# Kernel optimization log

Hardware: AMD Instinct MI355X
Metric: run time of the kernel (lower is better)

The kernel has to match this reference:

```python
import jax, jax.numpy as jnp
import numpy as np

EMB = 1024
HEADS = 8
HEAD_DIM = EMB // HEADS


def setup_inputs() -> dict:
    key = jax.random.key(0)
    ks = jax.random.split(key, 11)
    B, S = 4, 2048
    scale = 1.0 / np.sqrt(EMB)
    inp = {
        "query": jax.random.normal(ks[0], (B, S, EMB), jnp.float32),
        "key": jax.random.normal(ks[1], (B, S, EMB), jnp.float32),
        "value": jax.random.normal(ks[2], (B, S, EMB), jnp.float32),
        "Wq": jax.random.normal(ks[3], (EMB, EMB), jnp.float32) * scale,
        "bq": jnp.zeros((EMB,), jnp.float32),
        "Wk": jax.random.normal(ks[4], (EMB, EMB), jnp.float32) * scale,
        "bk": jnp.zeros((EMB,), jnp.float32),
        "Wv": jax.random.normal(ks[5], (EMB, EMB), jnp.float32) * scale,
        "bv": jnp.zeros((EMB,), jnp.float32),
        "Wo": jax.random.normal(ks[6], (EMB, EMB), jnp.float32) * scale,
        "bo": jnp.zeros((EMB,), jnp.float32),
    }
    return inp


def _split_heads(x):
    B, S, _ = x.shape
    return x.reshape(B, S, HEADS, HEAD_DIM).transpose(0, 2, 1, 3)  # [B,H,S,D]


def reference(query, key, value, Wq, bq, Wk, bk, Wv, bv, Wo, bo):
    Q = _split_heads(query @ Wq.T + bq)
    K = _split_heads(key @ Wk.T + bk)
    V = _split_heads(value @ Wv.T + bv)
    # [B,H,S,S] attention scores, scaled by sqrt(head_dim)
    scores = jnp.einsum("bhqd,bhkd->bhqk", Q, K) / jnp.sqrt(
        jnp.asarray(HEAD_DIM, Q.dtype)
    )
    attention = jax.nn.softmax(scores, axis=-1)
    # dropout is identity in eval mode
    x = jnp.einsum("bhqk,bhkd->bhqd", attention, V)
    B, H, S, D = x.shape
    x = x.transpose(0, 2, 1, 3).reshape(B, S, EMB)
    x = x @ Wo.T + bo
    return (x, attention)
```

## Files before the change

kernel.cpp:

```cpp
#include <hip/hip_runtime.h>
#include <hip/hip_bf16.h>
#include <math.h>

#define BB 4
#define SS 2048
#define EMB 1024
#define HH 8
#define DD 128

typedef __attribute__((ext_vector_type(8))) short bf16x8;
typedef __attribute__((ext_vector_type(4))) float f32x4;

__device__ __forceinline__ unsigned short f2bf(float f) {
    unsigned u = __builtin_bit_cast(unsigned, f);
    u += 0x7FFFu + ((u >> 16) & 1u);
    return (unsigned short)(u >> 16);
}

__device__ __forceinline__ void gload_lds16(const void* g, void* l) {
    __builtin_amdgcn_global_load_lds(
        (const __attribute__((address_space(1))) unsigned int*)g,
        (__attribute__((address_space(3))) unsigned int*)l, 16, 0, 0);
}

#define SB0 __builtin_amdgcn_sched_barrier(0)

__global__ void f2bf3_kernel(const float* __restrict__ a, const float* __restrict__ b,
                             const float* __restrict__ c, unsigned short* __restrict__ dst,
                             int n4) {
    const float* src = blockIdx.z == 0 ? a : (blockIdx.z == 1 ? b : c);
    unsigned short* d = dst + (size_t)blockIdx.z * ((size_t)n4 * 4);
    int i = blockIdx.x * blockDim.x + threadIdx.x;
    int stride = gridDim.x * blockDim.x;
    for (; i < n4; i += stride) {
        float4 f = ((const float4*)src)[i];
        ushort4 o;
        o.x = f2bf(f.x); o.y = f2bf(f.y); o.z = f2bf(f.z); o.w = f2bf(f.w);
        ((ushort4*)d)[i] = o;
    }
}

__global__ void f2bf4_kernel(const float* __restrict__ a, const float* __restrict__ b,
                             const float* __restrict__ c, const float* __restrict__ e,
                             unsigned short* __restrict__ dst, int n4) {
    const float* src = blockIdx.z == 0 ? a : (blockIdx.z == 1 ? b : (blockIdx.z == 2 ? c : e));
    unsigned short* d = dst + (size_t)blockIdx.z * ((size_t)n4 * 4);
    int i = blockIdx.x * blockDim.x + threadIdx.x;
    int stride = gridDim.x * blockDim.x;
    for (; i < n4; i += stride) {
        float4 f = ((const float4*)src)[i];
        ushort4 o;
        o.x = f2bf(f.x); o.y = f2bf(f.y); o.z = f2bf(f.z); o.w = f2bf(f.w);
        ((ushort4*)d)[i] = o;
    }
}

template <int MODE>
__device__ __forceinline__ void gemm_core(const unsigned short* __restrict__ A,
                                          const unsigned short* __restrict__ Bw,
                                          const float* __restrict__ bias,
                                          void* __restrict__ Cout, float scale)
{
    __shared__ short As[2][128 * 32];
    __shared__ short Bs[2][128 * 32];
    const int K = 1024;
    const int m0 = blockIdx.x * 128, n0 = blockIdx.y * 128;
    const int t = threadIdx.x;
    const int lane = t & 63, w = t >> 6;
    const int wr = w >> 1, wc = w & 1;
    const int g = lane >> 4, li = lane & 15;
    f32x4 acc[4][4] = {};

    auto stage = [&](int k0, int buf) {
        #pragma unroll
        for (int i = 0; i < 2; ++i) {
            int idx = i * 256 + t;
            int row = idx >> 2, col = (idx & 3) * 8;
            gload_lds16(A  + (size_t)(m0 + row) * K + k0 + col, &As[buf][idx * 8]);
            gload_lds16(Bw + (size_t)(n0 + row) * K + k0 + col, &Bs[buf][idx * 8]);
        }
    };

    stage(0, 0);
    for (int ki = 0; ki < 32; ++ki) {
        const int cur = ki & 1;
        if (ki < 31) {
            stage((ki + 1) * 32, cur ^ 1);
            asm volatile("s_waitcnt vmcnt(4)" ::: "memory");
        } else {
            asm volatile("s_waitcnt vmcnt(0)" ::: "memory");
        }
        SB0; __builtin_amdgcn_s_barrier(); SB0;

        bf16x8 af[4], bfr[4];
        #pragma unroll
        for (int mi = 0; mi < 4; ++mi)
            af[mi] = *(const bf16x8*)&As[cur][(wr * 64 + mi * 16 + li) * 32 + g * 8];
        #pragma unroll
        for (int ni = 0; ni < 4; ++ni)
            bfr[ni] = *(const bf16x8*)&Bs[cur][(wc * 64 + ni * 16 + li) * 32 + g * 8];
        #pragma unroll
        for (int mi = 0; mi < 4; ++mi) {
            #pragma unroll
            for (int ni = 0; ni < 4; ++ni)
                acc[mi][ni] = __builtin_amdgcn_mfma_f32_16x16x32_bf16(
                    af[mi], bfr[ni], acc[mi][ni], 0, 0, 0);
        }
        asm volatile("s_waitcnt lgkmcnt(0)" ::: "memory");
        SB0; __builtin_amdgcn_s_barrier(); SB0;
    }

    #pragma unroll
    for (int mi = 0; mi < 4; ++mi) {
        #pragma unroll
        for (int ni = 0; ni < 4; ++ni) {
            int n = n0 + wc * 64 + ni * 16 + li;
            float bv = bias[n];
            #pragma unroll
            for (int i = 0; i < 4; ++i) {
                int m = m0 + wr * 64 + mi * 16 + g * 4 + i;
                float v = acc[mi][ni][i] + bv;
                if (MODE == 0) {
                    v *= scale;
                    int b = m >> 11, s = m & 2047, h = n >> 7, d = n & 127;
                    ((unsigned short*)Cout)[((((size_t)b * HH + h) * SS + s) << 7) + d] = f2bf(v);
                } else {
                    ((float*)Cout)[(size_t)m * EMB + n] = v;
                }
            }
        }
    }
}

__global__ __launch_bounds__(256, 2)
void gemm_qkv(const unsigned short* __restrict__ XB, const unsigned short* __restrict__ WB,
              const float* __restrict__ bq, const float* __restrict__ bk,
              const float* __restrict__ bv, unsigned short* __restrict__ QKVb, float qscale)
{
    const size_t NX = (size_t)BB * SS * EMB;
    const size_t NW = (size_t)EMB * EMB;
    const int z = blockIdx.z;
    const float* bias = z == 0 ? bq : (z == 1 ? bk : bv);
    gemm_core<0>(XB + z * NX, WB + z * NW, bias, QKVb + z * NX, z == 0 ? qscale : 1.f);
}

__global__ __launch_bounds__(256, 2)
void gemm_out(const unsigned short* __restrict__ Ob, const unsigned short* __restrict__ Wo,
              const float* __restrict__ bo, float* __restrict__ outx)
{
    gemm_core<1>(Ob, Wo, bo, outx, 1.f);
}

__global__ __launch_bounds__(256, 2)
void attn_kernel(const unsigned short* __restrict__ Qb,
                 const unsigned short* __restrict__ Kb,
                 const unsigned short* __restrict__ Vb,
                 float* __restrict__ attn,
                 unsigned short* __restrict__ Ob)
{
    __shared__ short Ks[64 * 128];
    __shared__ short Vt[128 * 64];
    __shared__ short Ps[4][16 * 68];

    const int t = threadIdx.x;
    const int lane = t & 63, w = t >> 6;
    const int g = lane >> 4, li = lane & 15;
    const int bh = blockIdx.y;
    const int q0 = blockIdx.x * 64 + w * 16;

    const unsigned short* Kbh = Kb + (size_t)bh * SS * DD;
    const unsigned short* Vbh = Vb + (size_t)bh * SS * DD;

    bf16x8 qf[4];
    {
        const unsigned short* qp = Qb + ((size_t)bh * SS + q0 + li) * DD + g * 8;
        #pragma unroll
        for (int kk = 0; kk < 4; ++kk) qf[kk] = *(const bf16x8*)(qp + kk * 32);
    }

    float l_i[4] = {0.f, 0.f, 0.f, 0.f};

    auto stageK = [&](int kt2, char* dst) {
        const char* ksrc = (const char*)(Kbh + kt2 * 64 * DD);
        #pragma unroll
        for (int i = 0; i < 4; ++i) {
            int lb = (i * 256 + t) * 16;
            int row = lb >> 8;
            gload_lds16(ksrc + (lb ^ ((row & 7) << 4)), dst + lb);
        }
    };

    stageK(0, (char*)Ks);
    for (int kt = 0; kt < 32; ++kt) {
        const char* cur = (kt & 1) ? (const char*)Vt : (const char*)Ks;
        char* nxt = (kt & 1) ? (char*)Ks : (char*)Vt;
        if (kt < 31) {
            stageK(kt + 1, nxt);
            asm volatile("s_waitcnt vmcnt(4)" ::: "memory");
        } else {
            asm volatile("s_waitcnt vmcnt(0)" ::: "memory");
        }
        SB0; __builtin_amdgcn_s_barrier(); SB0;

        f32x4 sacc[4];
        #pragma unroll
        for (int kc = 0; kc < 4; ++kc) {
            f32x4 a = {0.f, 0.f, 0.f, 0.f};
            int row = kc * 16 + li;
            int sw = (row & 7) << 4;
            #pragma unroll
            for (int kk = 0; kk < 4; ++kk) {
                bf16x8 kf = *(const bf16x8*)(cur + row * 256 + ((kk * 64 + g * 16) ^ sw));
                a = __builtin_amdgcn_mfma_f32_16x16x32_bf16(qf[kk], kf, a, 0, 0, 0);
            }
            sacc[kc] = a;
        }
        #pragma unroll
        for (int i = 0; i < 4; ++i) {
            float ts = __builtin_amdgcn_exp2f(sacc[0][i]) + __builtin_amdgcn_exp2f(sacc[1][i])
                     + __builtin_amdgcn_exp2f(sacc[2][i]) + __builtin_amdgcn_exp2f(sacc[3][i]);
            #pragma unroll
            for (int mk = 1; mk < 16; mk <<= 1) ts += __shfl_xor(ts, mk, 64);
            l_i[i] += ts;
        }
        __builtin_amdgcn_s_barrier(); SB0;
    }

    float rl[4];
    #pragma unroll
    for (int i = 0; i < 4; ++i) rl[i] = 1.f / l_i[i];

    f32x4 O[8] = {};
    float* arow = attn + (size_t)bh * SS * SS;

    bf16x8 va[2], vbr[2];
    #pragma unroll
    for (int i = 0; i < 2; ++i) {
        int idx = i * 256 + t;
        int k0 = (idx >> 4) * 2, d0 = (idx & 15) * 8;
        va[i]  = *(const bf16x8*)(Vbh + k0 * DD + d0);
        vbr[i] = *(const bf16x8*)(Vbh + (k0 + 1) * DD + d0);
    }

    for (int kt = 0; kt < 32; ++kt) {
        __syncthreads();
        const char* ksrc = (const char*)(Kbh + kt * 64 * DD);
        #pragma unroll
        for (int i = 0; i < 4; ++i) {
            int lb = (i * 256 + t) * 16;
            int row = lb >> 8;
            gload_lds16(ksrc + (lb ^ ((row & 7) << 4)), (char*)Ks + lb);
        }
        #pragma unroll
        for (int i = 0; i < 2; ++i) {
            int idx = i * 256 + t;
            int kpair = idx >> 4, d0 = (idx & 15) * 8;
            #pragma unroll
            for (int j = 0; j < 8; ++j) {
                unsigned pk = (unsigned)(unsigned short)va[i][j]
                            | ((unsigned)(unsigned short)vbr[i][j] << 16);
                int d = d0 + j;
                int ba = (d * 128 + kpair * 4) ^ (((d >> 3) & 7) << 4);
                *(unsigned*)((char*)Vt + ba) = pk;
            }
        }
        __syncthreads();

        if (kt < 31) {
            const unsigned short* vn = Vbh + (kt + 1) * 64 * DD;
            #pragma unroll
            for (int i = 0; i < 2; ++i) {
                int idx = i * 256 + t;
                int k0 = (idx >> 4) * 2, d0 = (idx & 15) * 8;
                va[i]  = *(const bf16x8*)(vn + k0 * DD + d0);
                vbr[i] = *(const bf16x8*)(vn + (k0 + 1) * DD + d0);
            }
        }

        #pragma unroll
        for (int kc = 0; kc < 4; ++kc) {
            f32x4 a = {0.f, 0.f, 0.f, 0.f};
            int row = kc * 16 + li;
            int sw = (row & 7) << 4;
            #pragma unroll
            for (int kk = 0; kk < 4; ++kk) {
                bf16x8 kf = *(const bf16x8*)((const char*)Ks + row * 256 + ((kk * 64 + g * 16) ^ sw));
                a = __builtin_amdgcn_mfma_f32_16x16x32_bf16(qf[kk], kf, a, 0, 0, 0);
            }
            #pragma unroll
            for (int i = 0; i < 4; ++i) {
                float p = __builtin_amdgcn_exp2f(a[i]) * rl[i];
                int qr = g * 4 + i;
                __builtin_nontemporal_store(p, &arow[(size_t)(q0 + qr) * SS + kt * 64 + kc * 16 + li]);
                Ps[w][qr * 68 + kc * 16 + li] = (short)f2bf(p);
            }
        }
        asm volatile("s_waitcnt lgkmcnt(0)" ::: "memory");
        SB0;

        bf16x8 pf0 = *(const bf16x8*)&Ps[w][li * 68 + g * 8];
        bf16x8 pf1 = *(const bf16x8*)&Ps[w][li * 68 + 32 + g * 8];
        #pragma unroll
        for (int dt = 0; dt < 8; ++dt) {
            int dr = dt * 16 + li;
            int vsw = ((dr >> 3) & 7) << 4;
            bf16x8 vf0 = *(const bf16x8*)((const char*)Vt + dr * 128 + ((g * 16) ^ vsw));
            bf16x8 vf1 = *(const bf16x8*)((const char*)Vt + dr * 128 + ((64 + g * 16) ^ vsw));
            O[dt] = __builtin_amdgcn_mfma_f32_16x16x32_bf16(pf0, vf0, O[dt], 0, 0, 0);
            O[dt] = __builtin_amdgcn_mfma_f32_16x16x32_bf16(pf1, vf1, O[dt], 0, 0, 0);
        }
    }

    const int b = bh >> 3, h = bh & 7;
    #pragma unroll
    for (int dt = 0; dt < 8; ++dt) {
        #pragma unroll
        for (int i = 0; i < 4; ++i) {
            size_t r = (size_t)b * SS + q0 + g * 4 + i;
            Ob[r * EMB + h * DD + dt * 16 + li] = f2bf(O[dt][i]);
        }
    }
}

extern "C" void kernel_launch(void* const* d_in, const int* in_sizes, int n_in,
                              void* d_out, int out_size, void* d_ws, size_t ws_size,
                              hipStream_t stream)
{
    const float* q  = (const float*)d_in[0];
    const float* k  = (const float*)d_in[1];
    const float* v  = (const float*)d_in[2];
    const float* Wq = (const float*)d_in[3];
    const float* bq = (const float*)d_in[4];
    const float* Wk = (const float*)d_in[5];
    const float* bk = (const float*)d_in[6];
    const float* Wv = (const float*)d_in[7];
    const float* bv = (const float*)d_in[8];
    const float* Wo = (const float*)d_in[9];
    const float* bo = (const float*)d_in[10];

    const size_t NX = (size_t)BB * SS * EMB;
    const size_t NW = (size_t)EMB * EMB;

    unsigned short* Qb = (unsigned short*)d_ws;
    unsigned short* Ob = Qb + 3 * NX;
    unsigned short* WB = Ob + NX;

    float* outx = (float*)d_out;
    float* attn = outx + NX;
    unsigned short* XB = (unsigned short*)attn;

    f2bf3_kernel<<<dim3(1024, 1, 3), 256, 0, stream>>>(q, k, v, XB, (int)(NX / 4));
    f2bf4_kernel<<<dim3(128, 1, 4), 256, 0, stream>>>(Wq, Wk, Wv, Wo, WB, (int)(NW / 4));

    const float qscale = 1.4426950408889634f / sqrtf((float)DD);
    gemm_qkv<<<dim3(64, 8, 3), 256, 0, stream>>>(XB, WB, bq, bk, bv, Qb, qscale);

    attn_kernel<<<dim3(32, 32), 256, 0, stream>>>(Qb, Qb + NX, Qb + 2 * NX, attn, Ob);

    gemm_out<<<dim3(64, 8), 256, 0, stream>>>(Ob, WB + 3 * NW, bo, outx);
}
```

Before: 356.3 us.

## Process 32 query rows per wave in attention to reuse K/V tiles

Each wave now handles two 16-row query subtiles (128 queries per block), so every K and V tile staged in LDS feeds twice as many MFMAs, and the grid shrinks to 512 blocks. The softmax row sums are accumulated per lane and cross-lane reduced only once after the first pass, instead of every tile. Block ids are remapped so that consecutive blocks spread across batch-heads. This raises register pressure (more accumulators and Q fragments), which could hurt occupancy under the 2-blocks-per-SM launch bound.

```diff
diff --git a/kernel.cpp b/kernel.cpp
--- a/kernel.cpp
+++ b/kernel.cpp
@@ -160,25 +160,28 @@
 {
     __shared__ short Ks[64 * 128];
     __shared__ short Vt[128 * 64];
-    __shared__ short Ps[4][16 * 68];
+    __shared__ short Ps[4][32 * 68];
 
     const int t = threadIdx.x;
     const int lane = t & 63, w = t >> 6;
     const int g = lane >> 4, li = lane & 15;
-    const int bh = blockIdx.y;
-    const int q0 = blockIdx.x * 64 + w * 16;
+
+    const int id = blockIdx.x + blockIdx.y * 16;
+    const int bh = (id & 7) * 4 + ((id >> 3) & 3);
+    const int q0 = (id >> 5) * 128 + w * 32;
 
     const unsigned short* Kbh = Kb + (size_t)bh * SS * DD;
     const unsigned short* Vbh = Vb + (size_t)bh * SS * DD;
 
-    bf16x8 qf[4];
-    {
-        const unsigned short* qp = Qb + ((size_t)bh * SS + q0 + li) * DD + g * 8;
-        #pragma unroll
-        for (int kk = 0; kk < 4; ++kk) qf[kk] = *(const bf16x8*)(qp + kk * 32);
-    }
-
-    float l_i[4] = {0.f, 0.f, 0.f, 0.f};
+    bf16x8 qf[8];
+    #pragma unroll
+    for (int rh = 0; rh < 2; ++rh) {
+        const unsigned short* qp = Qb + ((size_t)bh * SS + q0 + rh * 16 + li) * DD + g * 8;
+        #pragma unroll
+        for (int kk = 0; kk < 4; ++kk) qf[rh * 4 + kk] = *(const bf16x8*)(qp + kk * 32);
+    }
+
+    float lacc[8] = {0.f, 0.f, 0.f, 0.f, 0.f, 0.f, 0.f, 0.f};
 
     auto stageK = [&](int kt2, char* dst) {
         const char* ksrc = (const char*)(Kbh + kt2 * 64 * DD);
@@ -202,35 +205,36 @@
         }
         SB0; __builtin_amdgcn_s_barrier(); SB0;
 
-        f32x4 sacc[4];
         #pragma unroll
         for (int kc = 0; kc < 4; ++kc) {
-            f32x4 a = {0.f, 0.f, 0.f, 0.f};
             int row = kc * 16 + li;
             int sw = (row & 7) << 4;
+            f32x4 a0 = {0.f, 0.f, 0.f, 0.f}, a1 = {0.f, 0.f, 0.f, 0.f};
             #pragma unroll
             for (int kk = 0; kk < 4; ++kk) {
                 bf16x8 kf = *(const bf16x8*)(cur + row * 256 + ((kk * 64 + g * 16) ^ sw));
-                a = __builtin_amdgcn_mfma_f32_16x16x32_bf16(qf[kk], kf, a, 0, 0, 0);
-            }
-            sacc[kc] = a;
-        }
-        #pragma unroll
-        for (int i = 0; i < 4; ++i) {
-            float ts = __builtin_amdgcn_exp2f(sacc[0][i]) + __builtin_amdgcn_exp2f(sacc[1][i])
-                     + __builtin_amdgcn_exp2f(sacc[2][i]) + __builtin_amdgcn_exp2f(sacc[3][i]);
-            #pragma unroll
-            for (int mk = 1; mk < 16; mk <<= 1) ts += __shfl_xor(ts, mk, 64);
-            l_i[i] += ts;
+                a0 = __builtin_amdgcn_mfma_f32_16x16x32_bf16(qf[kk],     kf, a0, 0, 0, 0);
+                a1 = __builtin_amdgcn_mfma_f32_16x16x32_bf16(qf[4 + kk], kf, a1, 0, 0, 0);
+            }
+            #pragma unroll
+            for (int i = 0; i < 4; ++i) {
+                lacc[i]     += __builtin_amdgcn_exp2f(a0[i]);
+                lacc[4 + i] += __builtin_amdgcn_exp2f(a1[i]);
+            }
         }
         __builtin_amdgcn_s_barrier(); SB0;
     }
 
-    float rl[4];
-    #pragma unroll
-    for (int i = 0; i < 4; ++i) rl[i] = 1.f / l_i[i];
-
-    f32x4 O[8] = {};
+    float rl[8];
+    #pragma unroll
+    for (int i = 0; i < 8; ++i) {
+        float ts = lacc[i];
+        #pragma unroll
+        for (int mk = 1; mk < 16; mk <<= 1) ts += __shfl_xor(ts, mk, 64);
+        rl[i] = 1.f / ts;
+    }
+
+    f32x4 O[16] = {};
     float* arow = attn + (size_t)bh * SS * SS;
 
     bf16x8 va[2], vbr[2];
@@ -279,20 +283,24 @@
 
         #pragma unroll
         for (int kc = 0; kc < 4; ++kc) {
-            f32x4 a = {0.f, 0.f, 0.f, 0.f};
             int row = kc * 16 + li;
             int sw = (row & 7) << 4;
+            f32x4 a0 = {0.f, 0.f, 0.f, 0.f}, a1 = {0.f, 0.f, 0.f, 0.f};
             #pragma unroll
             for (int kk = 0; kk < 4; ++kk) {
                 bf16x8 kf = *(const bf16x8*)((const char*)Ks + row * 256 + ((kk * 64 + g * 16) ^ sw));
-                a = __builtin_amdgcn_mfma_f32_16x16x32_bf16(qf[kk], kf, a, 0, 0, 0);
+                a0 = __builtin_amdgcn_mfma_f32_16x16x32_bf16(qf[kk],     kf, a0, 0, 0, 0);
+                a1 = __builtin_amdgcn_mfma_f32_16x16x32_bf16(qf[4 + kk], kf, a1, 0, 0, 0);
             }
             #pragma unroll
             for (int i = 0; i < 4; ++i) {
-                float p = __builtin_amdgcn_exp2f(a[i]) * rl[i];
-                int qr = g * 4 + i;
-                __builtin_nontemporal_store(p, &arow[(size_t)(q0 + qr) * SS + kt * 64 + kc * 16 + li]);
-                Ps[w][qr * 68 + kc * 16 + li] = (short)f2bf(p);
+                float p0 = __builtin_amdgcn_exp2f(a0[i]) * rl[i];
+                float p1 = __builtin_amdgcn_exp2f(a1[i]) * rl[4 + i];
+                int qr0 = g * 4 + i, qr1 = 16 + qr0;
+                __builtin_nontemporal_store(p0, &arow[(size_t)(q0 + qr0) * SS + kt * 64 + kc * 16 + li]);
+                __builtin_nontemporal_store(p1, &arow[(size_t)(q0 + qr1) * SS + kt * 64 + kc * 16 + li]);
+                Ps[w][qr0 * 68 + kc * 16 + li] = (short)f2bf(p0);
+                Ps[w][qr1 * 68 + kc * 16 + li] = (short)f2bf(p1);
             }
         }
         asm volatile("s_waitcnt lgkmcnt(0)" ::: "memory");
@@ -300,24 +308,31 @@
 
         bf16x8 pf0 = *(const bf16x8*)&Ps[w][li * 68 + g * 8];
         bf16x8 pf1 = *(const bf16x8*)&Ps[w][li * 68 + 32 + g * 8];
+        bf16x8 pf2 = *(const bf16x8*)&Ps[w][(16 + li) * 68 + g * 8];
+        bf16x8 pf3 = *(const bf16x8*)&Ps[w][(16 + li) * 68 + 32 + g * 8];
         #pragma unroll
         for (int dt = 0; dt < 8; ++dt) {
             int dr = dt * 16 + li;
             int vsw = ((dr >> 3) & 7) << 4;
             bf16x8 vf0 = *(const bf16x8*)((const char*)Vt + dr * 128 + ((g * 16) ^ vsw));
             bf16x8 vf1 = *(const bf16x8*)((const char*)Vt + dr * 128 + ((64 + g * 16) ^ vsw));
-            O[dt] = __builtin_amdgcn_mfma_f32_16x16x32_bf16(pf0, vf0, O[dt], 0, 0, 0);
-            O[dt] = __builtin_amdgcn_mfma_f32_16x16x32_bf16(pf1, vf1, O[dt], 0, 0, 0);
+            O[dt]     = __builtin_amdgcn_mfma_f32_16x16x32_bf16(pf0, vf0, O[dt],     0, 0, 0);
+            O[dt]     = __builtin_amdgcn_mfma_f32_16x16x32_bf16(pf1, vf1, O[dt],     0, 0, 0);
+            O[8 + dt] = __builtin_amdgcn_mfma_f32_16x16x32_bf16(pf2, vf0, O[8 + dt], 0, 0, 0);
+            O[8 + dt] = __builtin_amdgcn_mfma_f32_16x16x32_bf16(pf3, vf1, O[8 + dt], 0, 0, 0);
         }
     }
 
     const int b = bh >> 3, h = bh & 7;
     #pragma unroll
-    for (int dt = 0; dt < 8; ++dt) {
-        #pragma unroll
-        for (int i = 0; i < 4; ++i) {
-            size_t r = (size_t)b * SS + q0 + g * 4 + i;
-            Ob[r * EMB + h * DD + dt * 16 + li] = f2bf(O[dt][i]);
+    for (int rh = 0; rh < 2; ++rh) {
+        #pragma unroll
+        for (int dt = 0; dt < 8; ++dt) {
+            #pragma unroll
+            for (int i = 0; i < 4; ++i) {
+                size_t r = (size_t)b * SS + q0 + rh * 16 + g * 4 + i;
+                Ob[r * EMB + h * DD + dt * 16 + li] = f2bf(O[rh * 8 + dt][i]);
+            }
         }
     }
 }
@@ -355,7 +370,7 @@
     const float qscale = 1.4426950408889634f / sqrtf((float)DD);
     gemm_qkv<<<dim3(64, 8, 3), 256, 0, stream>>>(XB, WB, bq, bk, bv, Qb, qscale);
 
-    attn_kernel<<<dim3(32, 32), 256, 0, stream>>>(Qb, Qb + NX, Qb + 2 * NX, attn, Ob);
+    attn_kernel<<<dim3(16, 32), 256, 0, stream>>>(Qb, Qb + NX, Qb + 2 * NX, attn, Ob);
 
     gemm_out<<<dim3(64, 8), 256, 0, stream>>>(Ob, WB + 3 * NW, bo, outx);
 }
```

Result: slower. 379.9 us (+6.6%).

## Split softmax denominator pass into separate tiled QK^T sum-exp kernel

Applied to the files above, without the earlier changes.

Moves the first pass of attention, which computes the softmax row sums (sum of exp of QK^T), out of attn_kernel into a dedicated 128x128-tiled GEMM kernel. That kernel writes partial sums per column tile, and a small reduction kernel turns them into reciprocals. The large tiles give better MFMA reuse and more parallelism than the 16-row-per-wave streaming loop. The cost is two extra launches and a scratch buffer placed in the output region, which gemm_out later overwrites.

```diff
diff --git a/kernel.cpp b/kernel.cpp
--- a/kernel.cpp
+++ b/kernel.cpp
@@ -152,9 +152,91 @@
 }
 
 __global__ __launch_bounds__(256, 2)
+void qk_sumexp(const unsigned short* __restrict__ Qb,
+               const unsigned short* __restrict__ Kb,
+               float* __restrict__ lp)
+{
+    __shared__ short As[2][128 * 32];
+    __shared__ short Bs[2][128 * 32];
+    const int bh = blockIdx.z;
+    const int m0 = blockIdx.x * 128, n0 = blockIdx.y * 128;
+    const unsigned short* A  = Qb + (size_t)bh * SS * DD;
+    const unsigned short* Bw = Kb + (size_t)bh * SS * DD;
+    const int t = threadIdx.x;
+    const int lane = t & 63, w = t >> 6;
+    const int wr = w >> 1, wc = w & 1;
+    const int g = lane >> 4, li = lane & 15;
+    f32x4 acc[4][4] = {};
+
+    auto stage = [&](int k0, int buf) {
+        #pragma unroll
+        for (int i = 0; i < 2; ++i) {
+            int idx = i * 256 + t;
+            int row = idx >> 2, col = (idx & 3) * 8;
+            gload_lds16(A  + (size_t)(m0 + row) * DD + k0 + col, &As[buf][idx * 8]);
+            gload_lds16(Bw + (size_t)(n0 + row) * DD + k0 + col, &Bs[buf][idx * 8]);
+        }
+    };
+
+    stage(0, 0);
+    #pragma unroll
+    for (int ki = 0; ki < 4; ++ki) {
+        const int cur = ki & 1;
+        if (ki < 3) {
+            stage((ki + 1) * 32, cur ^ 1);
+            asm volatile("s_waitcnt vmcnt(4)" ::: "memory");
+        } else {
+            asm volatile("s_waitcnt vmcnt(0)" ::: "memory");
+        }
+        SB0; __builtin_amdgcn_s_barrier(); SB0;
+
+        bf16x8 af[4], bfr[4];
+        #pragma unroll
+        for (int mi = 0; mi < 4; ++mi)
+            af[mi] = *(const bf16x8*)&As[cur][(wr * 64 + mi * 16 + li) * 32 + g * 8];
+        #pragma unroll
+        for (int ni = 0; ni < 4; ++ni)
+            bfr[ni] = *(const bf16x8*)&Bs[cur][(wc * 64 + ni * 16 + li) * 32 + g * 8];
+        #pragma unroll
+        for (int mi = 0; mi < 4; ++mi) {
+            #pragma unroll
+            for (int ni = 0; ni < 4; ++ni)
+                acc[mi][ni] = __builtin_amdgcn_mfma_f32_16x16x32_bf16(
+                    af[mi], bfr[ni], acc[mi][ni], 0, 0, 0);
+        }
+        asm volatile("s_waitcnt lgkmcnt(0)" ::: "memory");
+        SB0; __builtin_amdgcn_s_barrier(); SB0;
+    }
+
+    #pragma unroll
+    for (int mi = 0; mi < 4; ++mi) {
+        #pragma unroll
+        for (int i = 0; i < 4; ++i) {
+            float s = __builtin_amdgcn_exp2f(acc[mi][0][i]) + __builtin_amdgcn_exp2f(acc[mi][1][i])
+                    + __builtin_amdgcn_exp2f(acc[mi][2][i]) + __builtin_amdgcn_exp2f(acc[mi][3][i]);
+            #pragma unroll
+            for (int mk = 1; mk < 16; mk <<= 1) s += __shfl_xor(s, mk, 64);
+            if (li == 0) {
+                int q = m0 + wr * 64 + mi * 16 + g * 4 + i;
+                lp[((size_t)bh * SS + q) * 32 + blockIdx.y * 2 + wc] = s;
+            }
+        }
+    }
+}
+
+__global__ void lred_kernel(const float* __restrict__ lp, float* __restrict__ rlg) {
+    int r = blockIdx.x * blockDim.x + threadIdx.x;
+    float s = 0.f;
+    #pragma unroll
+    for (int j = 0; j < 32; ++j) s += lp[(size_t)r * 32 + j];
+    rlg[r] = 1.f / s;
+}
+
+__global__ __launch_bounds__(256, 2)
 void attn_kernel(const unsigned short* __restrict__ Qb,
                  const unsigned short* __restrict__ Kb,
                  const unsigned short* __restrict__ Vb,
+                 const float* __restrict__ rlg,
                  float* __restrict__ attn,
                  unsigned short* __restrict__ Ob)
 {
@@ -178,57 +260,9 @@
         for (int kk = 0; kk < 4; ++kk) qf[kk] = *(const bf16x8*)(qp + kk * 32);
     }
 
-    float l_i[4] = {0.f, 0.f, 0.f, 0.f};
-
-    auto stageK = [&](int kt2, char* dst) {
-        const char* ksrc = (const char*)(Kbh + kt2 * 64 * DD);
-        #pragma unroll
-        for (int i = 0; i < 4; ++i) {
-            int lb = (i * 256 + t) * 16;
-            int row = lb >> 8;
-            gload_lds16(ksrc + (lb ^ ((row & 7) << 4)), dst + lb);
-        }
-    };
-
-    stageK(0, (char*)Ks);
-    for (int kt = 0; kt < 32; ++kt) {
-        const char* cur = (kt & 1) ? (const char*)Vt : (const char*)Ks;
-        char* nxt = (kt & 1) ? (char*)Ks : (char*)Vt;
-        if (kt < 31) {
-            stageK(kt + 1, nxt);
-            asm volatile("s_waitcnt vmcnt(4)" ::: "memory");
-        } else {
-            asm volatile("s_waitcnt vmcnt(0)" ::: "memory");
-        }
-        SB0; __builtin_amdgcn_s_barrier(); SB0;
-
-        f32x4 sacc[4];
-        #pragma unroll
-        for (int kc = 0; kc < 4; ++kc) {
-            f32x4 a = {0.f, 0.f, 0.f, 0.f};
-            int row = kc * 16 + li;
-            int sw = (row & 7) << 4;
-            #pragma unroll
-            for (int kk = 0; kk < 4; ++kk) {
-                bf16x8 kf = *(const bf16x8*)(cur + row * 256 + ((kk * 64 + g * 16) ^ sw));
-                a = __builtin_amdgcn_mfma_f32_16x16x32_bf16(qf[kk], kf, a, 0, 0, 0);
-            }
-            sacc[kc] = a;
-        }
-        #pragma unroll
-        for (int i = 0; i < 4; ++i) {
-            float ts = __builtin_amdgcn_exp2f(sacc[0][i]) + __builtin_amdgcn_exp2f(sacc[1][i])
-                     + __builtin_amdgcn_exp2f(sacc[2][i]) + __builtin_amdgcn_exp2f(sacc[3][i]);
-            #pragma unroll
-            for (int mk = 1; mk < 16; mk <<= 1) ts += __shfl_xor(ts, mk, 64);
-            l_i[i] += ts;
-        }
-        __builtin_amdgcn_s_barrier(); SB0;
-    }
-
     float rl[4];
     #pragma unroll
-    for (int i = 0; i < 4; ++i) rl[i] = 1.f / l_i[i];
+    for (int i = 0; i < 4; ++i) rl[i] = rlg[(size_t)bh * SS + q0 + g * 4 + i];
 
     f32x4 O[8] = {};
     float* arow = attn + (size_t)bh * SS * SS;
@@ -348,6 +382,8 @@
     float* outx = (float*)d_out;
     float* attn = outx + NX;
     unsigned short* XB = (unsigned short*)attn;
+    float* lp  = outx;
+    float* rlg = outx + 4 * 1024 * 1024;
 
     f2bf3_kernel<<<dim3(1024, 1, 3), 256, 0, stream>>>(q, k, v, XB, (int)(NX / 4));
     f2bf4_kernel<<<dim3(128, 1, 4), 256, 0, stream>>>(Wq, Wk, Wv, Wo, WB, (int)(NW / 4));
@@ -355,7 +391,10 @@
     const float qscale = 1.4426950408889634f / sqrtf((float)DD);
     gemm_qkv<<<dim3(64, 8, 3), 256, 0, stream>>>(XB, WB, bq, bk, bv, Qb, qscale);
 
-    attn_kernel<<<dim3(32, 32), 256, 0, stream>>>(Qb, Qb + NX, Qb + 2 * NX, attn, Ob);
+    qk_sumexp<<<dim3(16, 16, 32), 256, 0, stream>>>(Qb, Qb + NX, lp);
+    lred_kernel<<<dim3(256), 256, 0, stream>>>(lp, rlg);
+
+    attn_kernel<<<dim3(32, 32), 256, 0, stream>>>(Qb, Qb + NX, Qb + 2 * NX, rlg, attn, Ob);
 
     gemm_out<<<dim3(64, 8), 256, 0, stream>>>(Ob, WB + 3 * NW, bo, outx);
 }
```

New measurement: 413.8 us. 1.16x slower.

## Transpose QK MFMA operands so each lane owns one query row

Applied to the files above, without the earlier changes.

Swaps the A/B operands of the score MFMA so the accumulator is transposed and each lane holds four consecutive key columns of a single query row. This lets the row-sum be accumulated per lane with only two cross-group shuffles at the end instead of a 16-lane butterfly every tile. It also turns the four scalar attention-probability stores into one 16-byte nontemporal vector store and packs the bf16 conversion with v_cvt_pk_bf16_f32 into 8-byte LDS writes, with the P buffer padded to a 72-element stride. The cost is a new LDS layout and inline asm for the conversion, which changes rounding behaviour relative to the manual f2bf.

```diff
diff --git a/kernel.cpp b/kernel.cpp
--- a/kernel.cpp
+++ b/kernel.cpp
@@ -10,6 +10,7 @@
 
 typedef __attribute__((ext_vector_type(8))) short bf16x8;
 typedef __attribute__((ext_vector_type(4))) float f32x4;
+typedef __attribute__((ext_vector_type(2))) unsigned int u32x2;
 
 __device__ __forceinline__ unsigned short f2bf(float f) {
     unsigned u = __builtin_bit_cast(unsigned, f);
@@ -160,7 +161,7 @@
 {
     __shared__ short Ks[64 * 128];
     __shared__ short Vt[128 * 64];
-    __shared__ short Ps[4][16 * 68];
+    __shared__ short Ps[4][16 * 72];
 
     const int t = threadIdx.x;
     const int lane = t & 63, w = t >> 6;
@@ -178,7 +179,7 @@
         for (int kk = 0; kk < 4; ++kk) qf[kk] = *(const bf16x8*)(qp + kk * 32);
     }
 
-    float l_i[4] = {0.f, 0.f, 0.f, 0.f};
+    float lacc = 0.f;
 
     auto stageK = [&](int kt2, char* dst) {
         const char* ksrc = (const char*)(Kbh + kt2 * 64 * DD);
@@ -202,7 +203,6 @@
         }
         SB0; __builtin_amdgcn_s_barrier(); SB0;
 
-        f32x4 sacc[4];
         #pragma unroll
         for (int kc = 0; kc < 4; ++kc) {
             f32x4 a = {0.f, 0.f, 0.f, 0.f};
@@ -211,24 +211,18 @@
             #pragma unroll
             for (int kk = 0; kk < 4; ++kk) {
                 bf16x8 kf = *(const bf16x8*)(cur + row * 256 + ((kk * 64 + g * 16) ^ sw));
-                a = __builtin_amdgcn_mfma_f32_16x16x32_bf16(qf[kk], kf, a, 0, 0, 0);
-            }
-            sacc[kc] = a;
-        }
-        #pragma unroll
-        for (int i = 0; i < 4; ++i) {
-            float ts = __builtin_amdgcn_exp2f(sacc[0][i]) + __builtin_amdgcn_exp2f(sacc[1][i])
-                     + __builtin_amdgcn_exp2f(sacc[2][i]) + __builtin_amdgcn_exp2f(sacc[3][i]);
-            #pragma unroll
-            for (int mk = 1; mk < 16; mk <<= 1) ts += __shfl_xor(ts, mk, 64);
-            l_i[i] += ts;
+                a = __builtin_amdgcn_mfma_f32_16x16x32_bf16(kf, qf[kk], a, 0, 0, 0);
+            }
+            lacc += __builtin_amdgcn_exp2f(a[0]) + __builtin_amdgcn_exp2f(a[1])
+                  + __builtin_amdgcn_exp2f(a[2]) + __builtin_amdgcn_exp2f(a[3]);
         }
         __builtin_amdgcn_s_barrier(); SB0;
     }
 
-    float rl[4];
-    #pragma unroll
-    for (int i = 0; i < 4; ++i) rl[i] = 1.f / l_i[i];
+    float ts = lacc;
+    ts += __shfl_xor(ts, 16, 64);
+    ts += __shfl_xor(ts, 32, 64);
+    const float rl = 1.f / ts;
 
     f32x4 O[8] = {};
     float* arow = attn + (size_t)bh * SS * SS;
@@ -285,21 +279,26 @@
             #pragma unroll
             for (int kk = 0; kk < 4; ++kk) {
                 bf16x8 kf = *(const bf16x8*)((const char*)Ks + row * 256 + ((kk * 64 + g * 16) ^ sw));
-                a = __builtin_amdgcn_mfma_f32_16x16x32_bf16(qf[kk], kf, a, 0, 0, 0);
-            }
-            #pragma unroll
-            for (int i = 0; i < 4; ++i) {
-                float p = __builtin_amdgcn_exp2f(a[i]) * rl[i];
-                int qr = g * 4 + i;
-                __builtin_nontemporal_store(p, &arow[(size_t)(q0 + qr) * SS + kt * 64 + kc * 16 + li]);
-                Ps[w][qr * 68 + kc * 16 + li] = (short)f2bf(p);
-            }
+                a = __builtin_amdgcn_mfma_f32_16x16x32_bf16(kf, qf[kk], a, 0, 0, 0);
+            }
+            float p0 = __builtin_amdgcn_exp2f(a[0]) * rl;
+            float p1 = __builtin_amdgcn_exp2f(a[1]) * rl;
+            float p2 = __builtin_amdgcn_exp2f(a[2]) * rl;
+            float p3 = __builtin_amdgcn_exp2f(a[3]) * rl;
+            f32x4 pv = {p0, p1, p2, p3};
+            __builtin_nontemporal_store(pv,
+                (f32x4*)(arow + (size_t)(q0 + li) * SS + kt * 64 + kc * 16 + g * 4));
+            unsigned pk0, pk1;
+            asm("v_cvt_pk_bf16_f32 %0, %1, %2" : "=v"(pk0) : "v"(p0), "v"(p1));
+            asm("v_cvt_pk_bf16_f32 %0, %1, %2" : "=v"(pk1) : "v"(p2), "v"(p3));
+            u32x2 pw = {pk0, pk1};
+            *(u32x2*)((char*)&Ps[w][0] + li * 144 + kc * 32 + g * 8) = pw;
         }
         asm volatile("s_waitcnt lgkmcnt(0)" ::: "memory");
         SB0;
 
-        bf16x8 pf0 = *(const bf16x8*)&Ps[w][li * 68 + g * 8];
-        bf16x8 pf1 = *(const bf16x8*)&Ps[w][li * 68 + 32 + g * 8];
+        bf16x8 pf0 = *(const bf16x8*)((const char*)&Ps[w][0] + li * 144 + g * 16);
+        bf16x8 pf1 = *(const bf16x8*)((const char*)&Ps[w][0] + li * 144 + 64 + g * 16);
         #pragma unroll
         for (int dt = 0; dt < 8; ++dt) {
             int dr = dt * 16 + li;
```

Measured after the change: 355.3 us, median of 3. No clear change (-0.3%).
